# Optimization experiments

Hardware: AMD Instinct MI355X
Metric: run time of the kernel (lower is better)

The kernel has to match this reference:

```python
import jax, jax.numpy as jnp
import numpy as np

N_NODES = 50000


def _gcn_norm(edge_index, num_nodes):
    # add self-loops (PyG GCNConv default)
    loop = jnp.arange(num_nodes, dtype=edge_index.dtype)
    src = jnp.concatenate([edge_index[0], loop])
    dst = jnp.concatenate([edge_index[1], loop])
    deg = jax.ops.segment_sum(jnp.ones_like(dst, dtype=jnp.float32), dst,
                              num_segments=num_nodes)
    dis = jnp.where(deg > 0, jax.lax.rsqrt(deg), 0.0)  # deg^{-1/2}
    norm = dis[src] * dis[dst]                          # [E+N]
    return src, dst, norm


def _gcn_conv(x, W, b, src, dst, norm, num_nodes):
    h = x @ W                                   # [N, out] transform first
    msg = h[src] * norm[:, None]                # gather + scale  [E+N, out]
    out = jax.ops.segment_sum(msg, dst, num_segments=num_nodes)  # scatter-add
    return out + b


def setup_inputs() -> dict:
    key = jax.random.key(0)
    k1, k2, k3, k4, k5 = jax.random.split(key, 5)
    in_dim, hid_dim, out_dim = 128, 64, 2
    x = jax.random.normal(k1, (N_NODES, in_dim), dtype=jnp.float32)
    edge_index = jax.random.randint(k2, (2, 800000), 0, N_NODES, dtype=jnp.int64)
    s1 = 1.0 / np.sqrt(in_dim)
    s2 = 1.0 / np.sqrt(hid_dim)
    W1 = jax.random.uniform(k3, (in_dim, hid_dim), jnp.float32, -s1, s1)
    b1 = jnp.zeros((hid_dim,), jnp.float32)
    W2 = jax.random.uniform(k4, (hid_dim, hid_dim), jnp.float32, -s2, s2)
    b2 = jnp.zeros((hid_dim,), jnp.float32)
    Wl = jax.random.uniform(k5, (hid_dim, out_dim), jnp.float32, -s2, s2)
    bl = jnp.zeros((out_dim,), jnp.float32)
    return {"x": x, "edge_index": edge_index, "W1": W1, "b1": b1,
            "W2": W2, "b2": b2, "Wl": Wl, "bl": bl}


def reference(x, edge_index, W1, b1, W2, b2, Wl, bl):
    num_nodes = x.shape[0]
    src, dst, norm = _gcn_norm(edge_index, num_nodes)
    h = _gcn_conv(x, W1, b1, src, dst, norm, num_nodes)
    h = jax.nn.relu(h)
    # dropout is identity at inference
    h = _gcn_conv(h, W2, b2, src, dst, norm, num_nodes)
    h = jax.nn.relu(h)
    logits = h @ Wl + bl
    return logits
```

## Files before the change

### kernel.cpp

```cpp
#include <hip/hip_runtime.h>

#define IN_DIM 128
#define HID 64
#define STAGE_CAP 12288

__global__ __launch_bounds__(256) void k_bin_count(const int* __restrict__ dst, int E,
                                                   int* __restrict__ bcnt) {
    __shared__ int h[256];
    int tid = threadIdx.x;
    h[tid] = 0;
    __syncthreads();
    int base = blockIdx.x * 4096;
    int end = min(base + 4096, E);
    for (int i = base + tid; i < end; i += 256) atomicAdd(&h[dst[i] >> 8], 1);
    __syncthreads();
    if (h[tid]) atomicAdd(&bcnt[tid], h[tid]);
}

__global__ __launch_bounds__(256) void k_bucket_scan(const int* __restrict__ bcnt,
                                                     int* __restrict__ bbase,
                                                     int* __restrict__ gcur,
                                                     int* __restrict__ row_start, int N, int E) {
    int tid = threadIdx.x, lane = tid & 63, wid = tid >> 6;
    int v = bcnt[tid], orig = v;
    for (int off = 1; off < 64; off <<= 1) {
        int t = __shfl_up(v, off);
        if (lane >= off) v += t;
    }
    __shared__ int ws[4];
    if (lane == 63) ws[wid] = v;
    __syncthreads();
    int woff = 0;
    for (int w = 0; w < wid; ++w) woff += ws[w];
    bbase[tid] = woff + v - orig;
    gcur[tid] = 0;
    if (tid == 0) {
        bbase[256] = E;
        row_start[N] = E;
    }
}

__global__ __launch_bounds__(512) void k_bin_scatter(const int* __restrict__ src,
                                                     const int* __restrict__ dst, int E,
                                                     const int* __restrict__ bbase,
                                                     int* __restrict__ gcur,
                                                     unsigned* __restrict__ ebuf) {
    __shared__ int hist[256];
    __shared__ int gbase[256];
    int tid = threadIdx.x;
    for (int i = tid; i < 256; i += 512) hist[i] = 0;
    __syncthreads();
    int base = blockIdx.x * 4096;
    int pk[8], bkt[8], rnk[8];
#pragma unroll
    for (int i = 0; i < 8; ++i) {
        int e = base + tid + i * 512;
        if (e < E) {
            int s = src[e];
            int d = dst[e];
            bkt[i] = d >> 8;
            pk[i] = ((d & 255) << 16) | s;
            rnk[i] = atomicAdd(&hist[bkt[i]], 1);
        } else {
            bkt[i] = -1;
        }
    }
    __syncthreads();
    for (int b = tid; b < 256; b += 512) {
        int c = hist[b];
        if (c > 0) gbase[b] = bbase[b] + atomicAdd(&gcur[b], c);
    }
    __syncthreads();
#pragma unroll
    for (int i = 0; i < 8; ++i) {
        if (bkt[i] >= 0) ebuf[gbase[bkt[i]] + rnk[i]] = (unsigned)pk[i];
    }
}

__global__ __launch_bounds__(512) void k_bin_sort(const unsigned* __restrict__ ebuf,
                                                  const int* __restrict__ bbase, int N, int E,
                                                  int* __restrict__ row_start,
                                                  float* __restrict__ dis,
                                                  int* __restrict__ csr_src) {
    __shared__ int ldeg[256];
    __shared__ int loff[256];
    __shared__ int lcur[256];
    __shared__ int wsum[8];
    __shared__ unsigned short stage[STAGE_CAP];
    int tid = threadIdx.x;
    int node0 = blockIdx.x << 8;
    int nnode = min(256, N - node0);
    for (int i = tid; i < 256; i += 512) {
        ldeg[i] = 0;
        lcur[i] = 0;
    }
    __syncthreads();
    int bstart = bbase[blockIdx.x];
    int bend = bbase[blockIdx.x + 1];
    int cnt = bend - bstart;
    for (int i = tid; i < cnt; i += 512) {
        unsigned u = ebuf[bstart + i];
        atomicAdd(&ldeg[(u >> 16) & 255], 1);
    }
    __syncthreads();
    int lane = tid & 63, wid = tid >> 6;
    int v = 0, orig = 0;
    if (tid < 256) {
        orig = ldeg[tid];
        v = orig;
    }
    for (int off = 1; off < 64; off <<= 1) {
        int t = __shfl_up(v, off);
        if (lane >= off) v += t;
    }
    if (lane == 63) wsum[wid] = v;
    __syncthreads();
    if (tid < 256) {
        int woff = 0;
        for (int w = 0; w < wid && w < 4; ++w) woff += wsum[w];
        int excl = woff + v - orig;
        loff[tid] = excl;
        if (tid < nnode) {
            row_start[node0 + tid] = bstart + excl;
            dis[node0 + tid] = rsqrtf((float)(orig + 1));
        }
    }
    __syncthreads();
    if (cnt <= STAGE_CAP) {
        for (int i = tid; i < cnt; i += 512) {
            unsigned u = ebuf[bstart + i];
            int dlo = (u >> 16) & 255;
            int pos = loff[dlo] + atomicAdd(&lcur[dlo], 1);
            stage[pos] = (unsigned short)(u & 0xFFFF);
        }
        __syncthreads();
        for (int i = tid; i < cnt; i += 512) csr_src[bstart + i] = (int)stage[i];
    } else {
        for (int i = tid; i < cnt; i += 512) {
            unsigned u = ebuf[bstart + i];
            int dlo = (u >> 16) & 255;
            int pos = bstart + loff[dlo] + atomicAdd(&lcur[dlo], 1);
            csr_src[pos] = (int)(u & 0xFFFF);
        }
    }
}

template <int K>
__global__ __launch_bounds__(256) void k_gemm_scale(const float* __restrict__ X,
                                                    const float* __restrict__ W,
                                                    const float* __restrict__ dis, int N,
                                                    float* __restrict__ out) {
    constexpr int CH = 64;
    constexpr int CHP = CH + 4;
    constexpr int KC = K / 4;
    __shared__ float Xs[64 * CHP];
    __shared__ float Ws[CH * 64];
    int tid = threadIdx.x;
    int row0 = blockIdx.x * 64;
    int cg = tid & 15;
    int rg = tid >> 4;
    float acc[4][4] = {};
    const float4* Wg = (const float4*)W;
    const float4* Xg = (const float4*)X;
    float4* Ws4 = (float4*)Ws;

#pragma unroll
    for (int k0 = 0; k0 < K; k0 += CH) {
        if (k0) __syncthreads();
        for (int i = tid; i < CH * 16; i += 256) Ws4[i] = Wg[k0 * 16 + i];
        for (int c = tid; c < 64 * 16; c += 256) {
            int r = c >> 4, k4 = c & 15;
            int row = row0 + r;
            float4 vv = make_float4(0.f, 0.f, 0.f, 0.f);
            if (row < N) vv = Xg[(size_t)row * KC + (k0 >> 2) + k4];
            *(float4*)&Xs[r * CHP + k4 * 4] = vv;
        }
        __syncthreads();
#pragma unroll 2
        for (int k = 0; k < CH; k += 4) {
            float4 w0 = *(float4*)&Ws[(k + 0) * 64 + cg * 4];
            float4 w1 = *(float4*)&Ws[(k + 1) * 64 + cg * 4];
            float4 w2 = *(float4*)&Ws[(k + 2) * 64 + cg * 4];
            float4 w3 = *(float4*)&Ws[(k + 3) * 64 + cg * 4];
#pragma unroll
            for (int i = 0; i < 4; ++i) {
                float4 xv = *(float4*)&Xs[(rg * 4 + i) * CHP + k];
                acc[i][0] += xv.x * w0.x + xv.y * w1.x + xv.z * w2.x + xv.w * w3.x;
                acc[i][1] += xv.x * w0.y + xv.y * w1.y + xv.z * w2.y + xv.w * w3.y;
                acc[i][2] += xv.x * w0.z + xv.y * w1.z + xv.z * w2.z + xv.w * w3.z;
                acc[i][3] += xv.x * w0.w + xv.y * w1.w + xv.z * w2.w + xv.w * w3.w;
            }
        }
    }
#pragma unroll
    for (int i = 0; i < 4; ++i) {
        int row = row0 + rg * 4 + i;
        if (row < N) {
            float s = dis[row];
            *(float4*)&out[(size_t)row * 64 + cg * 4] =
                make_float4(acc[i][0] * s, acc[i][1] * s, acc[i][2] * s, acc[i][3] * s);
        }
    }
}

__global__ __launch_bounds__(256) void k_aggregate(const float* __restrict__ Hs,
                                                   const int* __restrict__ row_start,
                                                   const int* __restrict__ csr_src,
                                                   const float* __restrict__ dis,
                                                   const float* __restrict__ bias, int N,
                                                   float* __restrict__ out) {
    const float4* Hs4 = (const float4*)Hs;
    int wave = threadIdx.x >> 6, lane = threadIdx.x & 63;
    int node = blockIdx.x * 4 + wave;
    if (node >= N) return;
    int t = lane & 7, g = lane >> 3;
    float4 a0 = make_float4(0.f, 0.f, 0.f, 0.f);
    float4 a1 = a0;
    if (g == 0) {
        a0 = Hs4[(size_t)node * 16 + t];
        a1 = Hs4[(size_t)node * 16 + t + 8];
    }
    int e0 = row_start[node], e1 = row_start[node + 1];
    for (int eb = e0; eb < e1; eb += 64) {
        int cnt = min(64, e1 - eb);
        int sv = (eb + lane < e1) ? csr_src[eb + lane] : 0;
        for (int jb = 0; jb < cnt; jb += 32) {
            int i0 = jb + g, i1 = jb + 8 + g, i2 = jb + 16 + g, i3 = jb + 24 + g;
            int s0 = __shfl(sv, i0 < cnt ? i0 : 0);
            int s1 = __shfl(sv, i1 < cnt ? i1 : 0);
            int s2 = __shfl(sv, i2 < cnt ? i2 : 0);
            int s3 = __shfl(sv, i3 < cnt ? i3 : 0);
            size_t b0 = (size_t)s0 * 16, b1 = (size_t)s1 * 16;
            size_t b2 = (size_t)s2 * 16, b3 = (size_t)s3 * 16;
            float4 z00 = Hs4[b0 + t], z01 = Hs4[b0 + t + 8];
            float4 z10 = Hs4[b1 + t], z11 = Hs4[b1 + t + 8];
            float4 z20 = Hs4[b2 + t], z21 = Hs4[b2 + t + 8];
            float4 z30 = Hs4[b3 + t], z31 = Hs4[b3 + t + 8];
            if (i0 < cnt) {
                a0.x += z00.x; a0.y += z00.y; a0.z += z00.z; a0.w += z00.w;
                a1.x += z01.x; a1.y += z01.y; a1.z += z01.z; a1.w += z01.w;
            }
            if (i1 < cnt) {
                a0.x += z10.x; a0.y += z10.y; a0.z += z10.z; a0.w += z10.w;
                a1.x += z11.x; a1.y += z11.y; a1.z += z11.z; a1.w += z11.w;
            }
            if (i2 < cnt) {
                a0.x += z20.x; a0.y += z20.y; a0.z += z20.z; a0.w += z20.w;
                a1.x += z21.x; a1.y += z21.y; a1.z += z21.z; a1.w += z21.w;
            }
            if (i3 < cnt) {
                a0.x += z30.x; a0.y += z30.y; a0.z += z30.z; a0.w += z30.w;
                a1.x += z31.x; a1.y += z31.y; a1.z += z31.z; a1.w += z31.w;
            }
        }
    }
#pragma unroll
    for (int off = 8; off < 64; off <<= 1) {
        a0.x += __shfl_xor(a0.x, off); a0.y += __shfl_xor(a0.y, off);
        a0.z += __shfl_xor(a0.z, off); a0.w += __shfl_xor(a0.w, off);
        a1.x += __shfl_xor(a1.x, off); a1.y += __shfl_xor(a1.y, off);
        a1.z += __shfl_xor(a1.z, off); a1.w += __shfl_xor(a1.w, off);
    }
    float sc = dis[node];
    const float4* b4 = (const float4*)bias;
    float4 b0 = b4[t], b1 = b4[t + 8];
    float4 v0, v1;
    v0.x = fmaxf(a0.x * sc + b0.x, 0.f); v0.y = fmaxf(a0.y * sc + b0.y, 0.f);
    v0.z = fmaxf(a0.z * sc + b0.z, 0.f); v0.w = fmaxf(a0.w * sc + b0.w, 0.f);
    v1.x = fmaxf(a1.x * sc + b1.x, 0.f); v1.y = fmaxf(a1.y * sc + b1.y, 0.f);
    v1.z = fmaxf(a1.z * sc + b1.z, 0.f); v1.w = fmaxf(a1.w * sc + b1.w, 0.f);
    if (g == 0) {
        float4* o4 = (float4*)out;
        o4[(size_t)node * 16 + t] = v0;
        o4[(size_t)node * 16 + t + 8] = v1;
    }
}

__global__ __launch_bounds__(256) void k_aggregate_head(const float* __restrict__ Hs,
                                                        const int* __restrict__ row_start,
                                                        const int* __restrict__ csr_src,
                                                        const float* __restrict__ dis,
                                                        const float* __restrict__ bias,
                                                        const float* __restrict__ Wl,
                                                        const float* __restrict__ bl, int N,
                                                        float* __restrict__ out) {
    const float4* Hs4 = (const float4*)Hs;
    int wave = threadIdx.x >> 6, lane = threadIdx.x & 63;
    int node = blockIdx.x * 4 + wave;
    if (node >= N) return;
    int t = lane & 7, g = lane >> 3;
    float4 a0 = make_float4(0.f, 0.f, 0.f, 0.f);
    float4 a1 = a0;
    if (g == 0) {
        a0 = Hs4[(size_t)node * 16 + t];
        a1 = Hs4[(size_t)node * 16 + t + 8];
    }
    int e0 = row_start[node], e1 = row_start[node + 1];
    for (int eb = e0; eb < e1; eb += 64) {
        int cnt = min(64, e1 - eb);
        int sv = (eb + lane < e1) ? csr_src[eb + lane] : 0;
        for (int jb = 0; jb < cnt; jb += 32) {
            int i0 = jb + g, i1 = jb + 8 + g, i2 = jb + 16 + g, i3 = jb + 24 + g;
            int s0 = __shfl(sv, i0 < cnt ? i0 : 0);
            int s1 = __shfl(sv, i1 < cnt ? i1 : 0);
            int s2 = __shfl(sv, i2 < cnt ? i2 : 0);
            int s3 = __shfl(sv, i3 < cnt ? i3 : 0);
            size_t b0 = (size_t)s0 * 16, b1 = (size_t)s1 * 16;
            size_t b2 = (size_t)s2 * 16, b3 = (size_t)s3 * 16;
            float4 z00 = Hs4[b0 + t], z01 = Hs4[b0 + t + 8];
            float4 z10 = Hs4[b1 + t], z11 = Hs4[b1 + t + 8];
            float4 z20 = Hs4[b2 + t], z21 = Hs4[b2 + t + 8];
            float4 z30 = Hs4[b3 + t], z31 = Hs4[b3 + t + 8];
            if (i0 < cnt) {
                a0.x += z00.x; a0.y += z00.y; a0.z += z00.z; a0.w += z00.w;
                a1.x += z01.x; a1.y += z01.y; a1.z += z01.z; a1.w += z01.w;
            }
            if (i1 < cnt) {
                a0.x += z10.x; a0.y += z10.y; a0.z += z10.z; a0.w += z10.w;
                a1.x += z11.x; a1.y += z11.y; a1.z += z11.z; a1.w += z11.w;
            }
            if (i2 < cnt) {
                a0.x += z20.x; a0.y += z20.y; a0.z += z20.z; a0.w += z20.w;
                a1.x += z21.x; a1.y += z21.y; a1.z += z21.z; a1.w += z21.w;
            }
            if (i3 < cnt) {
                a0.x += z30.x; a0.y += z30.y; a0.z += z30.z; a0.w += z30.w;
                a1.x += z31.x; a1.y += z31.y; a1.z += z31.z; a1.w += z31.w;
            }
        }
    }
#pragma unroll
    for (int off = 8; off < 64; off <<= 1) {
        a0.x += __shfl_xor(a0.x, off); a0.y += __shfl_xor(a0.y, off);
        a0.z += __shfl_xor(a0.z, off); a0.w += __shfl_xor(a0.w, off);
        a1.x += __shfl_xor(a1.x, off); a1.y += __shfl_xor(a1.y, off);
        a1.z += __shfl_xor(a1.z, off); a1.w += __shfl_xor(a1.w, off);
    }
    float sc = dis[node];
    const float4* b4 = (const float4*)bias;
    float4 b0 = b4[t], b1 = b4[t + 8];
    float4 v0, v1;
    v0.x = fmaxf(a0.x * sc + b0.x, 0.f); v0.y = fmaxf(a0.y * sc + b0.y, 0.f);
    v0.z = fmaxf(a0.z * sc + b0.z, 0.f); v0.w = fmaxf(a0.w * sc + b0.w, 0.f);
    v1.x = fmaxf(a1.x * sc + b1.x, 0.f); v1.y = fmaxf(a1.y * sc + b1.y, 0.f);
    v1.z = fmaxf(a1.z * sc + b1.z, 0.f); v1.w = fmaxf(a1.w * sc + b1.w, 0.f);
    int c0 = 4 * t, c1 = 32 + 4 * t;
    float p0 = v0.x * Wl[(c0 + 0) * 2] + v0.y * Wl[(c0 + 1) * 2] +
               v0.z * Wl[(c0 + 2) * 2] + v0.w * Wl[(c0 + 3) * 2] +
               v1.x * Wl[(c1 + 0) * 2] + v1.y * Wl[(c1 + 1) * 2] +
               v1.z * Wl[(c1 + 2) * 2] + v1.w * Wl[(c1 + 3) * 2];
    float p1 = v0.x * Wl[(c0 + 0) * 2 + 1] + v0.y * Wl[(c0 + 1) * 2 + 1] +
               v0.z * Wl[(c0 + 2) * 2 + 1] + v0.w * Wl[(c0 + 3) * 2 + 1] +
               v1.x * Wl[(c1 + 0) * 2 + 1] + v1.y * Wl[(c1 + 1) * 2 + 1] +
               v1.z * Wl[(c1 + 2) * 2 + 1] + v1.w * Wl[(c1 + 3) * 2 + 1];
    p0 += __shfl_xor(p0, 1); p1 += __shfl_xor(p1, 1);
    p0 += __shfl_xor(p0, 2); p1 += __shfl_xor(p1, 2);
    p0 += __shfl_xor(p0, 4); p1 += __shfl_xor(p1, 4);
    if (lane == 0) {
        out[node * 2 + 0] = p0 + bl[0];
        out[node * 2 + 1] = p1 + bl[1];
    }
}

extern "C" void kernel_launch(void* const* d_in, const int* in_sizes, int n_in,
                              void* d_out, int out_size, void* d_ws, size_t ws_size,
                              hipStream_t stream) {
    const float* x  = (const float*)d_in[0];
    const int*   ei = (const int*)d_in[1];
    const float* W1 = (const float*)d_in[2];
    const float* b1 = (const float*)d_in[3];
    const float* W2 = (const float*)d_in[4];
    const float* b2 = (const float*)d_in[5];
    const float* Wl = (const float*)d_in[6];
    const float* bl = (const float*)d_in[7];

    const int N = in_sizes[0] / IN_DIM;
    const int E = in_sizes[1] / 2;
    const int* src = ei;
    const int* dst = ei + E;

    char* ws = (char*)d_ws;
    size_t off = 0;
    auto alloc = [&](size_t bytes) -> void* {
        void* p = ws + off;
        off = (off + bytes + 255) & ~(size_t)255;
        return p;
    };
    int*   bcnt      = (int*)alloc(256 * 4);
    int*   bbase     = (int*)alloc(257 * 4);
    int*   gcur      = (int*)alloc(256 * 4);
    int*   row_start = (int*)alloc(((size_t)N + 1) * 4);
    float* dis       = (float*)alloc((size_t)N * 4);
    int*   csr_src   = (int*)alloc((size_t)E * 4);
    float* bufA      = (float*)alloc((size_t)N * HID * 4);
    float* bufB      = (float*)alloc((size_t)N * HID * 4);
    unsigned* ebuf   = (unsigned*)bufA;

    hipMemsetAsync(bcnt, 0, 256 * 4, stream);

    int eblk = (E + 4095) / 4096;
    int nb = (N + 255) / 256;
    k_bin_count<<<eblk, 256, 0, stream>>>(dst, E, bcnt);
    k_bucket_scan<<<1, 256, 0, stream>>>(bcnt, bbase, gcur, row_start, N, E);
    k_bin_scatter<<<eblk, 512, 0, stream>>>(src, dst, E, bbase, gcur, ebuf);
    k_bin_sort<<<nb, 512, 0, stream>>>(ebuf, bbase, N, E, row_start, dis, csr_src);

    int gblk = (N + 63) / 64;
    int nblk = (N + 3) / 4;
    k_gemm_scale<IN_DIM><<<gblk, 256, 0, stream>>>(x, W1, dis, N, bufA);
    k_aggregate<<<nblk, 256, 0, stream>>>(bufA, row_start, csr_src, dis, b1, N, bufB);
    k_gemm_scale<HID><<<gblk, 256, 0, stream>>>(bufB, W2, dis, N, bufA);
    k_aggregate_head<<<nblk, 256, 0, stream>>>(bufA, row_start, csr_src, dis, b2, Wl, bl, N,
                                               (float*)d_out);
}
```

Before: 136.2 us.

## Split aggregation into column slices, separate head kernel, use per-block histograms

The aggregation kernel is restructured so that each block handles one 16-float column slice (64 bytes) for 16 nodes. Block indices are interleaved so the four slice passes over the same node group run close together in time, with the aim of improving cache locality and gather coalescing. The fused head is split into its own kernel, which adds an extra write and read of the hidden layer. The global atomic bin count is replaced by per-block histograms that a single-block scan sums, which removes the memset and the atomics but adds a serial reduction over all blocks in the scan.

```diff
diff --git a/kernel.cpp b/kernel.cpp
--- a/kernel.cpp
+++ b/kernel.cpp
@@ -5,7 +5,7 @@
 #define STAGE_CAP 12288
 
 __global__ __launch_bounds__(256) void k_bin_count(const int* __restrict__ dst, int E,
-                                                   int* __restrict__ bcnt) {
+                                                   int* __restrict__ hist2d) {
     __shared__ int h[256];
     int tid = threadIdx.x;
     h[tid] = 0;
@@ -14,15 +14,17 @@
     int end = min(base + 4096, E);
     for (int i = base + tid; i < end; i += 256) atomicAdd(&h[dst[i] >> 8], 1);
     __syncthreads();
-    if (h[tid]) atomicAdd(&bcnt[tid], h[tid]);
-}
-
-__global__ __launch_bounds__(256) void k_bucket_scan(const int* __restrict__ bcnt,
+    hist2d[blockIdx.x * 256 + tid] = h[tid];
+}
+
+__global__ __launch_bounds__(256) void k_bucket_scan(const int* __restrict__ hist2d, int eblk,
                                                      int* __restrict__ bbase,
                                                      int* __restrict__ gcur,
                                                      int* __restrict__ row_start, int N, int E) {
     int tid = threadIdx.x, lane = tid & 63, wid = tid >> 6;
-    int v = bcnt[tid], orig = v;
+    int v = 0;
+    for (int k = 0; k < eblk; ++k) v += hist2d[k * 256 + tid];
+    int orig = v;
     for (int off = 1; off < 64; off <<= 1) {
         int t = __shfl_up(v, off);
         if (lane >= off) v += t;
@@ -203,162 +205,76 @@
     }
 }
 
-__global__ __launch_bounds__(256) void k_aggregate(const float* __restrict__ Hs,
-                                                   const int* __restrict__ row_start,
-                                                   const int* __restrict__ csr_src,
-                                                   const float* __restrict__ dis,
-                                                   const float* __restrict__ bias, int N,
-                                                   float* __restrict__ out) {
+__global__ __launch_bounds__(1024) void k_agg_slice(const float* __restrict__ Hs,
+                                                    const int* __restrict__ row_start,
+                                                    const int* __restrict__ csr_src,
+                                                    const float* __restrict__ dis,
+                                                    const float* __restrict__ bias, int N,
+                                                    float* __restrict__ out) {
     const float4* Hs4 = (const float4*)Hs;
+    int blk = blockIdx.x;
+    int slot = blk & 7;
+    int pass = slot >> 1;
+    int idx = ((blk >> 3) << 1) | (slot & 1);
     int wave = threadIdx.x >> 6, lane = threadIdx.x & 63;
-    int node = blockIdx.x * 4 + wave;
+    int node = idx * 16 + wave;
     if (node >= N) return;
-    int t = lane & 7, g = lane >> 3;
-    float4 a0 = make_float4(0.f, 0.f, 0.f, 0.f);
-    float4 a1 = a0;
-    if (g == 0) {
-        a0 = Hs4[(size_t)node * 16 + t];
-        a1 = Hs4[(size_t)node * 16 + t + 8];
-    }
+    int t = lane & 3, g = lane >> 2;
+    int cbase = pass * 4;
+    float4 a = make_float4(0.f, 0.f, 0.f, 0.f);
+    if (g == 0) a = Hs4[(size_t)node * 16 + cbase + t];
     int e0 = row_start[node], e1 = row_start[node + 1];
     for (int eb = e0; eb < e1; eb += 64) {
         int cnt = min(64, e1 - eb);
         int sv = (eb + lane < e1) ? csr_src[eb + lane] : 0;
         for (int jb = 0; jb < cnt; jb += 32) {
-            int i0 = jb + g, i1 = jb + 8 + g, i2 = jb + 16 + g, i3 = jb + 24 + g;
+            int i0 = jb + g, i1 = jb + 16 + g;
             int s0 = __shfl(sv, i0 < cnt ? i0 : 0);
             int s1 = __shfl(sv, i1 < cnt ? i1 : 0);
-            int s2 = __shfl(sv, i2 < cnt ? i2 : 0);
-            int s3 = __shfl(sv, i3 < cnt ? i3 : 0);
-            size_t b0 = (size_t)s0 * 16, b1 = (size_t)s1 * 16;
-            size_t b2 = (size_t)s2 * 16, b3 = (size_t)s3 * 16;
-            float4 z00 = Hs4[b0 + t], z01 = Hs4[b0 + t + 8];
-            float4 z10 = Hs4[b1 + t], z11 = Hs4[b1 + t + 8];
-            float4 z20 = Hs4[b2 + t], z21 = Hs4[b2 + t + 8];
-            float4 z30 = Hs4[b3 + t], z31 = Hs4[b3 + t + 8];
+            float4 z0 = Hs4[(size_t)s0 * 16 + cbase + t];
+            float4 z1 = Hs4[(size_t)s1 * 16 + cbase + t];
             if (i0 < cnt) {
-                a0.x += z00.x; a0.y += z00.y; a0.z += z00.z; a0.w += z00.w;
-                a1.x += z01.x; a1.y += z01.y; a1.z += z01.z; a1.w += z01.w;
+                a.x += z0.x; a.y += z0.y; a.z += z0.z; a.w += z0.w;
             }
             if (i1 < cnt) {
-                a0.x += z10.x; a0.y += z10.y; a0.z += z10.z; a0.w += z10.w;
-                a1.x += z11.x; a1.y += z11.y; a1.z += z11.z; a1.w += z11.w;
+                a.x += z1.x; a.y += z1.y; a.z += z1.z; a.w += z1.w;
             }
-            if (i2 < cnt) {
-                a0.x += z20.x; a0.y += z20.y; a0.z += z20.z; a0.w += z20.w;
-                a1.x += z21.x; a1.y += z21.y; a1.z += z21.z; a1.w += z21.w;
-            }
-            if (i3 < cnt) {
-                a0.x += z30.x; a0.y += z30.y; a0.z += z30.z; a0.w += z30.w;
-                a1.x += z31.x; a1.y += z31.y; a1.z += z31.z; a1.w += z31.w;
-            }
-        }
-    }
-#pragma unroll
-    for (int off = 8; off < 64; off <<= 1) {
-        a0.x += __shfl_xor(a0.x, off); a0.y += __shfl_xor(a0.y, off);
-        a0.z += __shfl_xor(a0.z, off); a0.w += __shfl_xor(a0.w, off);
-        a1.x += __shfl_xor(a1.x, off); a1.y += __shfl_xor(a1.y, off);
-        a1.z += __shfl_xor(a1.z, off); a1.w += __shfl_xor(a1.w, off);
+        }
+    }
+#pragma unroll
+    for (int off = 4; off < 64; off <<= 1) {
+        a.x += __shfl_xor(a.x, off);
+        a.y += __shfl_xor(a.y, off);
+        a.z += __shfl_xor(a.z, off);
+        a.w += __shfl_xor(a.w, off);
     }
     float sc = dis[node];
-    const float4* b4 = (const float4*)bias;
-    float4 b0 = b4[t], b1 = b4[t + 8];
-    float4 v0, v1;
-    v0.x = fmaxf(a0.x * sc + b0.x, 0.f); v0.y = fmaxf(a0.y * sc + b0.y, 0.f);
-    v0.z = fmaxf(a0.z * sc + b0.z, 0.f); v0.w = fmaxf(a0.w * sc + b0.w, 0.f);
-    v1.x = fmaxf(a1.x * sc + b1.x, 0.f); v1.y = fmaxf(a1.y * sc + b1.y, 0.f);
-    v1.z = fmaxf(a1.z * sc + b1.z, 0.f); v1.w = fmaxf(a1.w * sc + b1.w, 0.f);
-    if (g == 0) {
-        float4* o4 = (float4*)out;
-        o4[(size_t)node * 16 + t] = v0;
-        o4[(size_t)node * 16 + t + 8] = v1;
-    }
-}
-
-__global__ __launch_bounds__(256) void k_aggregate_head(const float* __restrict__ Hs,
-                                                        const int* __restrict__ row_start,
-                                                        const int* __restrict__ csr_src,
-                                                        const float* __restrict__ dis,
-                                                        const float* __restrict__ bias,
-                                                        const float* __restrict__ Wl,
-                                                        const float* __restrict__ bl, int N,
-                                                        float* __restrict__ out) {
-    const float4* Hs4 = (const float4*)Hs;
+    float4 b = ((const float4*)bias)[cbase + t];
+    float4 v;
+    v.x = fmaxf(a.x * sc + b.x, 0.f);
+    v.y = fmaxf(a.y * sc + b.y, 0.f);
+    v.z = fmaxf(a.z * sc + b.z, 0.f);
+    v.w = fmaxf(a.w * sc + b.w, 0.f);
+    if (g == 0) ((float4*)out)[(size_t)node * 16 + cbase + t] = v;
+}
+
+__global__ __launch_bounds__(256) void k_head(const float* __restrict__ H,
+                                              const float* __restrict__ Wl,
+                                              const float* __restrict__ bl, int N,
+                                              float* __restrict__ out) {
     int wave = threadIdx.x >> 6, lane = threadIdx.x & 63;
     int node = blockIdx.x * 4 + wave;
     if (node >= N) return;
-    int t = lane & 7, g = lane >> 3;
-    float4 a0 = make_float4(0.f, 0.f, 0.f, 0.f);
-    float4 a1 = a0;
-    if (g == 0) {
-        a0 = Hs4[(size_t)node * 16 + t];
-        a1 = Hs4[(size_t)node * 16 + t + 8];
-    }
-    int e0 = row_start[node], e1 = row_start[node + 1];
-    for (int eb = e0; eb < e1; eb += 64) {
-        int cnt = min(64, e1 - eb);
-        int sv = (eb + lane < e1) ? csr_src[eb + lane] : 0;
-        for (int jb = 0; jb < cnt; jb += 32) {
-            int i0 = jb + g, i1 = jb + 8 + g, i2 = jb + 16 + g, i3 = jb + 24 + g;
-            int s0 = __shfl(sv, i0 < cnt ? i0 : 0);
-            int s1 = __shfl(sv, i1 < cnt ? i1 : 0);
-            int s2 = __shfl(sv, i2 < cnt ? i2 : 0);
-            int s3 = __shfl(sv, i3 < cnt ? i3 : 0);
-            size_t b0 = (size_t)s0 * 16, b1 = (size_t)s1 * 16;
-            size_t b2 = (size_t)s2 * 16, b3 = (size_t)s3 * 16;
-            float4 z00 = Hs4[b0 + t], z01 = Hs4[b0 + t + 8];
-            float4 z10 = Hs4[b1 + t], z11 = Hs4[b1 + t + 8];
-            float4 z20 = Hs4[b2 + t], z21 = Hs4[b2 + t + 8];
-            float4 z30 = Hs4[b3 + t], z31 = Hs4[b3 + t + 8];
-            if (i0 < cnt) {
-                a0.x += z00.x; a0.y += z00.y; a0.z += z00.z; a0.w += z00.w;
-                a1.x += z01.x; a1.y += z01.y; a1.z += z01.z; a1.w += z01.w;
-            }
-            if (i1 < cnt) {
-                a0.x += z10.x; a0.y += z10.y; a0.z += z10.z; a0.w += z10.w;
-                a1.x += z11.x; a1.y += z11.y; a1.z += z11.z; a1.w += z11.w;
-            }
-            if (i2 < cnt) {
-                a0.x += z20.x; a0.y += z20.y; a0.z += z20.z; a0.w += z20.w;
-                a1.x += z21.x; a1.y += z21.y; a1.z += z21.z; a1.w += z21.w;
-            }
-            if (i3 < cnt) {
-                a0.x += z30.x; a0.y += z30.y; a0.z += z30.z; a0.w += z30.w;
-                a1.x += z31.x; a1.y += z31.y; a1.z += z31.z; a1.w += z31.w;
-            }
-        }
-    }
-#pragma unroll
-    for (int off = 8; off < 64; off <<= 1) {
-        a0.x += __shfl_xor(a0.x, off); a0.y += __shfl_xor(a0.y, off);
-        a0.z += __shfl_xor(a0.z, off); a0.w += __shfl_xor(a0.w, off);
-        a1.x += __shfl_xor(a1.x, off); a1.y += __shfl_xor(a1.y, off);
-        a1.z += __shfl_xor(a1.z, off); a1.w += __shfl_xor(a1.w, off);
-    }
-    float sc = dis[node];
-    const float4* b4 = (const float4*)bias;
-    float4 b0 = b4[t], b1 = b4[t + 8];
-    float4 v0, v1;
-    v0.x = fmaxf(a0.x * sc + b0.x, 0.f); v0.y = fmaxf(a0.y * sc + b0.y, 0.f);
-    v0.z = fmaxf(a0.z * sc + b0.z, 0.f); v0.w = fmaxf(a0.w * sc + b0.w, 0.f);
-    v1.x = fmaxf(a1.x * sc + b1.x, 0.f); v1.y = fmaxf(a1.y * sc + b1.y, 0.f);
-    v1.z = fmaxf(a1.z * sc + b1.z, 0.f); v1.w = fmaxf(a1.w * sc + b1.w, 0.f);
-    int c0 = 4 * t, c1 = 32 + 4 * t;
-    float p0 = v0.x * Wl[(c0 + 0) * 2] + v0.y * Wl[(c0 + 1) * 2] +
-               v0.z * Wl[(c0 + 2) * 2] + v0.w * Wl[(c0 + 3) * 2] +
-               v1.x * Wl[(c1 + 0) * 2] + v1.y * Wl[(c1 + 1) * 2] +
-               v1.z * Wl[(c1 + 2) * 2] + v1.w * Wl[(c1 + 3) * 2];
-    float p1 = v0.x * Wl[(c0 + 0) * 2 + 1] + v0.y * Wl[(c0 + 1) * 2 + 1] +
-               v0.z * Wl[(c0 + 2) * 2 + 1] + v0.w * Wl[(c0 + 3) * 2 + 1] +
-               v1.x * Wl[(c1 + 0) * 2 + 1] + v1.y * Wl[(c1 + 1) * 2 + 1] +
-               v1.z * Wl[(c1 + 2) * 2 + 1] + v1.w * Wl[(c1 + 3) * 2 + 1];
-    p0 += __shfl_xor(p0, 1); p1 += __shfl_xor(p1, 1);
-    p0 += __shfl_xor(p0, 2); p1 += __shfl_xor(p1, 2);
-    p0 += __shfl_xor(p0, 4); p1 += __shfl_xor(p1, 4);
+    float h = H[(size_t)node * HID + lane];
+    float a0 = h * Wl[lane * 2 + 0];
+    float a1 = h * Wl[lane * 2 + 1];
+    for (int off = 32; off; off >>= 1) {
+        a0 += __shfl_down(a0, off);
+        a1 += __shfl_down(a1, off);
+    }
     if (lane == 0) {
-        out[node * 2 + 0] = p0 + bl[0];
-        out[node * 2 + 1] = p1 + bl[1];
+        out[node * 2 + 0] = a0 + bl[0];
+        out[node * 2 + 1] = a1 + bl[1];
     }
 }
 
@@ -386,7 +302,9 @@
         off = (off + bytes + 255) & ~(size_t)255;
         return p;
     };
-    int*   bcnt      = (int*)alloc(256 * 4);
+    const int eblk = (E + 4095) / 4096;
+    const int nb = (N + 255) / 256;
+    int*   hist2d    = (int*)alloc((size_t)eblk * 256 * 4);
     int*   bbase     = (int*)alloc(257 * 4);
     int*   gcur      = (int*)alloc(256 * 4);
     int*   row_start = (int*)alloc(((size_t)N + 1) * 4);
@@ -396,20 +314,19 @@
     float* bufB      = (float*)alloc((size_t)N * HID * 4);
     unsigned* ebuf   = (unsigned*)bufA;
 
-    hipMemsetAsync(bcnt, 0, 256 * 4, stream);
-
-    int eblk = (E + 4095) / 4096;
-    int nb = (N + 255) / 256;
-    k_bin_count<<<eblk, 256, 0, stream>>>(dst, E, bcnt);
-    k_bucket_scan<<<1, 256, 0, stream>>>(bcnt, bbase, gcur, row_start, N, E);
+    k_bin_count<<<eblk, 256, 0, stream>>>(dst, E, hist2d);
+    k_bucket_scan<<<1, 256, 0, stream>>>(hist2d, eblk, bbase, gcur, row_start, N, E);
     k_bin_scatter<<<eblk, 512, 0, stream>>>(src, dst, E, bbase, gcur, ebuf);
     k_bin_sort<<<nb, 512, 0, stream>>>(ebuf, bbase, N, E, row_start, dis, csr_src);
 
-    int gblk = (N + 63) / 64;
-    int nblk = (N + 3) / 4;
+    const int gblk = (N + 63) / 64;
+    const int nodeBlocks = (N + 15) / 16;
+    const int aggGrid = ((nodeBlocks + 1) / 2) * 8;
+    const int hblk = (N + 3) / 4;
+
     k_gemm_scale<IN_DIM><<<gblk, 256, 0, stream>>>(x, W1, dis, N, bufA);
-    k_aggregate<<<nblk, 256, 0, stream>>>(bufA, row_start, csr_src, dis, b1, N, bufB);
+    k_agg_slice<<<aggGrid, 1024, 0, stream>>>(bufA, row_start, csr_src, dis, b1, N, bufB);
     k_gemm_scale<HID><<<gblk, 256, 0, stream>>>(bufB, W2, dis, N, bufA);
-    k_aggregate_head<<<nblk, 256, 0, stream>>>(bufA, row_start, csr_src, dis, b2, Wl, bl, N,
-                                               (float*)d_out);
-}
+    k_agg_slice<<<aggGrid, 1024, 0, stream>>>(bufA, row_start, csr_src, dis, b2, N, bufB);
+    k_head<<<hblk, 256, 0, stream>>>(bufB, Wl, bl, N, (float*)d_out);
+}
```

Measured after the change: 235.8 us. 1.73x slower.
